# Performance work log

Measured on AMD Instinct MI355X. Metric: run time of the kernel, lower is better.

Reference implementation:

```python
import jax, jax.numpy as jnp
import numpy as np

B, T, C = 128, 384, 256
H, KV, D = 4, 2, 64          # n_head, n_kv_head, head_dim
REP = H // KV                # query heads per kv head
BLOCK_SIZE = 384


def setup_inputs() -> dict:
    key = jax.random.key(0)
    k0, k1, k2, k3, k4 = jax.random.split(key, 5)
    scale = 0.02
    return {
        "x":  jax.random.normal(k0, (B, T, C), jnp.float32),
        "Wq": jax.random.normal(k1, (C, H * D), jnp.float32) * scale,
        "Wk": jax.random.normal(k2, (C, KV * D), jnp.float32) * scale,
        "Wv": jax.random.normal(k3, (C, KV * D), jnp.float32) * scale,
        "Wo": jax.random.normal(k4, (C, C), jnp.float32) * scale,
    }


def _rope_tables(t_len):
    inv_freq = 1.0 / (10000.0 ** (jnp.arange(0, D, 2, dtype=jnp.float32) / D))
    t = jnp.arange(t_len, dtype=jnp.float32)
    freqs = jnp.outer(t, inv_freq)            # [T, D/2]
    emb = jnp.concatenate([freqs, freqs], -1)  # [T, D]
    return jnp.cos(emb), jnp.sin(emb)


def _rotate_half(x):
    h = x.shape[-1] // 2
    return jnp.concatenate([-x[..., h:], x[..., :h]], -1)


def _apply_rope(x, cos, sin):
    # x: [B, heads, T, D]; cos/sin: [T, D]
    return x * cos[None, None] + _rotate_half(x) * sin[None, None]


def reference(x, Wq, Wk, Wv, Wo):
    b, t, c = x.shape
    q = (x @ Wq).reshape(b, t, H, D).transpose(0, 2, 1, 3)   # [B,H,T,D]
    k = (x @ Wk).reshape(b, t, KV, D).transpose(0, 2, 1, 3)  # [B,KV,T,D]
    v = (x @ Wv).reshape(b, t, KV, D).transpose(0, 2, 1, 3)

    cos, sin = _rope_tables(t)
    q = _apply_rope(q, cos, sin)
    k = _apply_rope(k, cos, sin)

    # GQA: group query heads by kv head instead of repeat_interleave on K/V.
    qg = q.reshape(b, KV, REP, t, D)
    scores = jnp.einsum('bgrtd,bgsd->bgrts', qg, k) / jnp.sqrt(jnp.float32(D))
    causal = jnp.tril(jnp.ones((t, t), dtype=bool))
    scores = jnp.where(causal, scores, jnp.finfo(scores.dtype).min)
    p = jax.nn.softmax(scores, axis=-1)
    y = jnp.einsum('bgrts,bgsd->bgrtd', p, v)                 # [B,KV,REP,T,D]
    y = y.reshape(b, H, t, D).transpose(0, 2, 1, 3).reshape(b, t, c)
    return y @ Wo
```

## Files before the change

### kernel.cpp

```cpp
#include <hip/hip_runtime.h>
#include <hip/hip_bf16.h>

#define BB 128
#define TT 384
#define CC 256
#define HH 4
#define KVH 2
#define QKVW 512
#define MROWS (BB * TT)

typedef __attribute__((ext_vector_type(8))) short short8;
typedef __attribute__((ext_vector_type(4))) float float4v;

__device__ __forceinline__ unsigned short f2b(float f) {
    union { float f; unsigned u; } v; v.f = f;
    unsigned u = v.u;
    unsigned r = (u + 0x7fffu + ((u >> 16) & 1u)) >> 16;
    return (unsigned short)r;
}
__device__ __forceinline__ float4v mfma16(short8 a, short8 b, float4v c) {
    return __builtin_amdgcn_mfma_f32_16x16x32_bf16(a, b, c, 0, 0, 0);
}
__device__ __forceinline__ void g2lds16(const void* g, void* l) {
    __builtin_amdgcn_global_load_lds(
        (const __attribute__((address_space(1))) unsigned int*)g,
        (__attribute__((address_space(3))) unsigned int*)l, 16, 0, 0);
}
__device__ __forceinline__ unsigned pk2bf(float a, float b) {
    union { float f; unsigned u; } x, y; x.f = a; y.f = b;
    return __builtin_amdgcn_perm(y.u + 0x8000u, x.u + 0x8000u, 0x07060302u);
}

__global__ void prep_kernel(const float* __restrict__ Wq, const float* __restrict__ Wk,
                            const float* __restrict__ Wv, const float* __restrict__ Wo,
                            unsigned short* __restrict__ WqkvT, unsigned short* __restrict__ WoT,
                            float* __restrict__ cosT, float* __restrict__ sinT) {
    int idx = blockIdx.x * 256 + threadIdx.x;
    const int N1 = QKVW * CC;
    const int N2 = N1 + CC * CC;
    const int N3 = N2 + TT * 32;
    if (idx < N1) {
        int n = idx >> 8, k = idx & 255;
        float w;
        if (n < 256)      w = Wq[k * 256 + n];
        else if (n < 384) w = Wk[k * 128 + (n - 256)];
        else              w = Wv[k * 128 + (n - 384)];
        WqkvT[n * 256 + k] = f2b(w);
    } else if (idx < N2) {
        int i = idx - N1; int n = i >> 8, k = i & 255;
        WoT[n * 256 + k] = f2b(Wo[k * 256 + n]);
    } else if (idx < N3) {
        int i = idx - N2;
        int t = i >> 5, f = i & 31;
        double invf = exp2(-(double)f / 32.0 * 13.287712379549449);
        double ang = (double)t * invf;
        cosT[t * 32 + f] = (float)cos(ang);
        sinT[t * 32 + f] = (float)sin(ang);
    }
}

__global__ __launch_bounds__(256) void gemm_qkv_kernel(
    const float* __restrict__ X, const unsigned short* __restrict__ BT,
    unsigned short* __restrict__ Qr, unsigned short* __restrict__ Kr,
    unsigned short* __restrict__ Vt,
    const float* __restrict__ cosT, const float* __restrict__ sinT)
{
    __shared__ __align__(16) unsigned short As[2][128 * 32];
    __shared__ __align__(16) unsigned short Bs[2][128 * 32];
    const int tid  = threadIdx.x;
    const int lane = tid & 63;
    const int quad = lane >> 4, l16 = lane & 15;
    const int wave = tid >> 6;
    const int mt = ((blockIdx.x >> 5) << 3) | (blockIdx.x & 7);
    const int nt = (blockIdx.x >> 3) & 3;
    const int mbase = mt * 128, nbase = nt * 128;
    const int wmb = (wave >> 1) * 64, wnb = (wave & 1) * 64;

    float4v acc[4][4] = {};
    const int r0 = tid >> 2, kc = (tid & 3) * 8;
    const int ldsW = (tid & ~63) * 16;
    const float*          gX0 = X  + (size_t)(mbase + r0) * CC + kc;
    const unsigned short* gB0 = BT + (size_t)(nbase + r0) * CC + kc;

    float4 a0, a1, a2, a3;
    auto loadA = [&](int kt) {
        const float4* p0 = (const float4*)(gX0 + kt);
        const float4* p1 = (const float4*)(gX0 + kt + (size_t)64 * CC);
        a0 = p0[0]; a1 = p0[1]; a2 = p1[0]; a3 = p1[1];
    };
    auto writeA = [&](int bi) {
        short8 w0, w1;
        w0[0]=(short)f2b(a0.x); w0[1]=(short)f2b(a0.y); w0[2]=(short)f2b(a0.z); w0[3]=(short)f2b(a0.w);
        w0[4]=(short)f2b(a1.x); w0[5]=(short)f2b(a1.y); w0[6]=(short)f2b(a1.z); w0[7]=(short)f2b(a1.w);
        w1[0]=(short)f2b(a2.x); w1[1]=(short)f2b(a2.y); w1[2]=(short)f2b(a2.z); w1[3]=(short)f2b(a2.w);
        w1[4]=(short)f2b(a3.x); w1[5]=(short)f2b(a3.y); w1[6]=(short)f2b(a3.z); w1[7]=(short)f2b(a3.w);
        *(short8*)&As[bi][r0 * 32 + kc]        = w0;
        *(short8*)&As[bi][(r0 + 64) * 32 + kc] = w1;
    };
    auto stageB = [&](int bi, int kt) {
        g2lds16(gB0 + kt,                  (char*)&Bs[bi][0] + ldsW);
        g2lds16(gB0 + kt + (size_t)64*CC,  (char*)&Bs[bi][0] + 4096 + ldsW);
    };

    loadA(0);
    stageB(0, 0);
    writeA(0);
    for (int ks = 0; ks < 8; ks++) {
        __syncthreads();
        if (ks < 7) { loadA((ks + 1) * 32); stageB((ks + 1) & 1, (ks + 1) * 32); }
        const unsigned short* Ac = &As[ks & 1][0];
        const unsigned short* Bc = &Bs[ks & 1][0];

        short8 af[4], bf_[4];
        #pragma unroll
        for (int i = 0; i < 4; i++)
            af[i] = *(const short8*)&Ac[(wmb + i * 16 + l16) * 32 + quad * 8];
        #pragma unroll
        for (int i = 0; i < 4; i++)
            bf_[i] = *(const short8*)&Bc[(wnb + i * 16 + l16) * 32 + quad * 8];
        #pragma unroll
        for (int i = 0; i < 4; i++)
            #pragma unroll
            for (int j = 0; j < 4; j++)
                acc[i][j] = mfma16(af[i], bf_[j], acc[i][j]);

        if (ks < 7) writeA((ks + 1) & 1);
    }

    const int gn0 = nbase + wnb;
    const int gm0 = mbase + wmb;
    if (gn0 < 384) {
        const bool isq = (gn0 < 256);
        const int  hh  = isq ? (gn0 >> 6) : ((gn0 - 256) >> 6);
        const float qs = isq ? 0.18033688011112042f : 1.0f;
        #pragma unroll
        for (int i = 0; i < 4; i++) {
            #pragma unroll
            for (int r = 0; r < 4; r++) {
                int gm = gm0 + i * 16 + quad * 4 + r;
                int b = gm / TT, t = gm - b * TT;
                unsigned short* dst = isq
                    ? (Qr + (((size_t)b * HH  + hh) * TT + t) * 64)
                    : (Kr + (((size_t)b * KVH + hh) * TT + t) * 64);
                #pragma unroll
                for (int j = 0; j < 2; j++) {
                    int f = j * 16 + l16;
                    float cs = cosT[t * 32 + f], sn = sinT[t * 32 + f];
                    float a  = acc[i][j][r],     c2 = acc[i][j + 2][r];
                    dst[f]      = f2b((a * cs - c2 * sn) * qs);
                    dst[f + 32] = f2b((c2 * cs + a * sn) * qs);
                }
            }
        }
    } else {
        const int g = (gn0 - 384) >> 6;
        #pragma unroll
        for (int i = 0; i < 4; i++) {
            #pragma unroll
            for (int r = 0; r < 4; r++) {
                int gm = gm0 + i * 16 + quad * 4 + r;
                int b = gm / TT, s = gm - b * TT;
                int s6 = s & 63;
                int sig = (s6 & 15) * 4 + (s6 >> 4);
                unsigned short* dst = Vt + (((size_t)b * KVH + g) * 6 + (s >> 6)) * 4096 + sig;
                #pragma unroll
                for (int j = 0; j < 4; j++)
                    dst[(j * 16 + l16) * 64] = f2b(acc[i][j][r]);
            }
        }
    }
}

__global__ __launch_bounds__(256) void gemm_out_kernel(
    const unsigned short* __restrict__ A, const unsigned short* __restrict__ BT,
    float* __restrict__ C)
{
    __shared__ __align__(16) unsigned short As[2][128 * 32];
    __shared__ __align__(16) unsigned short Bs[2][128 * 32];
    const int tid  = threadIdx.x;
    const int lane = tid & 63;
    const int quad = lane >> 4, l16 = lane & 15;
    const int wave = tid >> 6;
    const int mt = ((blockIdx.x >> 4) << 3) | (blockIdx.x & 7);
    const int nt = (blockIdx.x >> 3) & 1;
    const int mbase = mt * 128, nbase = nt * 128;
    const int wmb = (wave >> 1) * 64, wnb = (wave & 1) * 64;

    float4v acc[4][4] = {};
    const int r0 = tid >> 2, kc = (tid & 3) * 8;
    const int ldsW = (tid & ~63) * 16;
    const unsigned short* gA0 = A  + (size_t)(mbase + r0) * CC + kc;
    const unsigned short* gB0 = BT + (size_t)(nbase + r0) * CC + kc;

    auto stage = [&](int bi, int kt) {
        g2lds16(gA0 + kt,                  (char*)&As[bi][0] + ldsW);
        g2lds16(gA0 + kt + (size_t)64*CC,  (char*)&As[bi][0] + 4096 + ldsW);
        g2lds16(gB0 + kt,                  (char*)&Bs[bi][0] + ldsW);
        g2lds16(gB0 + kt + (size_t)64*CC,  (char*)&Bs[bi][0] + 4096 + ldsW);
    };

    stage(0, 0);
    for (int ks = 0; ks < 8; ks++) {
        __syncthreads();
        if (ks < 7) stage((ks + 1) & 1, (ks + 1) * 32);
        const unsigned short* Ac = &As[ks & 1][0];
        const unsigned short* Bc = &Bs[ks & 1][0];

        short8 af[4], bf_[4];
        #pragma unroll
        for (int i = 0; i < 4; i++)
            af[i] = *(const short8*)&Ac[(wmb + i * 16 + l16) * 32 + quad * 8];
        #pragma unroll
        for (int i = 0; i < 4; i++)
            bf_[i] = *(const short8*)&Bc[(wnb + i * 16 + l16) * 32 + quad * 8];
        #pragma unroll
        for (int i = 0; i < 4; i++)
            #pragma unroll
            for (int j = 0; j < 4; j++)
                acc[i][j] = mfma16(af[i], bf_[j], acc[i][j]);
    }
    #pragma unroll
    for (int i = 0; i < 4; i++)
        #pragma unroll
        for (int j = 0; j < 4; j++)
            #pragma unroll
            for (int r = 0; r < 4; r++)
                C[(size_t)(mbase + wmb + i * 16 + quad * 4 + r) * CC + nbase + wnb + j * 16 + l16]
                    = acc[i][j][r];
}

__global__ __launch_bounds__(256, 3) void attn_kernel(
    const unsigned short* __restrict__ Qr, const unsigned short* __restrict__ Kr,
    const unsigned short* __restrict__ Vt, unsigned short* __restrict__ y)
{
    __shared__ __align__(16) unsigned short Ks[2][64 * 64];
    __shared__ __align__(16) unsigned short Vs[2][64 * 64];
    __shared__ __align__(16) unsigned short Ps[4][32 * 64];

    const int tid  = threadIdx.x;
    const int lane = tid & 63;
    const int wave = tid >> 6;
    const int quad = lane >> 4, l16 = lane & 15;

    const int xc  = blockIdx.x & 7;
    const int jj  = blockIdx.x >> 3;
    const int p   = jj % 3;
    const int bg  = (jj / 3) * 8 + xc;
    const int g   = bg & 1, b = bg >> 1;
    const int h   = g * 2 + (wave >> 1);

    const unsigned short* Kbase = Kr + ((size_t)b * KVH + g) * TT * 64;
    const unsigned short* Vbase = Vt + ((size_t)b * KVH + g) * 6 * 4096;
    const unsigned short* Qbase = Qr + ((size_t)b * HH + h) * TT * 64;
    unsigned short* ybase = y + (size_t)b * TT * CC + h * 64;
    char* Pw = (char*)&Ps[wave][0];
    const int ldsWave = (tid & ~63) * 16;
    int gc0, gc1;
    { int L0 = tid;       gc0 = ((L0 & ~7) | ((L0 & 7) ^ ((L0 >> 3) & 7))) * 8;
      int L1 = 256 + tid; gc1 = ((L1 & ~7) | ((L1 & 7) ^ ((L1 >> 3) & 7))) * 8; }

    auto stage = [&](int bi, int kt) {
        const unsigned short* kB = Kbase + (size_t)kt * 4096;
        const unsigned short* vB = Vbase + (size_t)kt * 4096;
        g2lds16(kB + gc0, (char*)&Ks[bi][0] + ldsWave);
        g2lds16(kB + gc1, (char*)&Ks[bi][0] + 4096 + ldsWave);
        g2lds16(vB + gc0, (char*)&Vs[bi][0] + ldsWave);
        g2lds16(vB + gc1, (char*)&Vs[bi][0] + 4096 + ldsWave);
    };

    short8 ones;
    #pragma unroll
    for (int j = 0; j < 8; j++) ones[j] = (short)0x3F80;

    int seq = 0;
    stage(0, 0);

    for (int tph = 0; tph < 2; tph++) {
        const int qt = tph ? (5 - p) : p;
        const int qb = qt * 64 + (wave & 1) * 32;

        short8 qf[2][2];
        #pragma unroll
        for (int mi = 0; mi < 2; mi++)
            #pragma unroll
            for (int half = 0; half < 2; half++)
                qf[mi][half] = *(const short8*)(Qbase
                    + (size_t)(qb + mi * 16 + l16) * 64 + half * 32 + quad * 8);

        float4v acc[2][4] = {};
        float4v accl[2]   = {};

        for (int kt = 0; kt <= qt; kt++) {
            __syncthreads();
            if (kt < qt)        stage((seq + 1) & 1, kt + 1);
            else if (tph == 0)  stage((seq + 1) & 1, 0);
            const unsigned short* Kc = &Ks[seq & 1][0];
            const unsigned short* Vc = &Vs[seq & 1][0];

            float4v s_[2][4];
            #pragma unroll
            for (int js = 0; js < 4; js++) {
                int srow = js * 16 + l16, sw = srow & 7;
                short8 kb0 = *(const short8*)((const char*)Kc + srow * 128 + ((quad ^ sw) * 16));
                short8 kb1 = *(const short8*)((const char*)Kc + srow * 128 + (((4 + quad) ^ sw) * 16));
                #pragma unroll
                for (int mi = 0; mi < 2; mi++) {
                    float4v z = {};
                    z = mfma16(qf[mi][0], kb0, z);
                    s_[mi][js] = mfma16(qf[mi][1], kb1, z);
                }
            }

            if (kt == qt) {
                #pragma unroll
                for (int mi = 0; mi < 2; mi++)
                    #pragma unroll
                    for (int js = 0; js < 4; js++) {
                        int coll = js * 16 + l16;
                        #pragma unroll
                        for (int r = 0; r < 4; r++) {
                            int rowl = (wave & 1) * 32 + mi * 16 + quad * 4 + r;
                            if (coll > rowl) s_[mi][js][r] = -1e30f;
                        }
                    }
            }

            #pragma unroll
            for (int mi = 0; mi < 2; mi++)
                #pragma unroll
                for (int r = 0; r < 4; r++) {
                    float e0 = __builtin_amdgcn_exp2f(s_[mi][0][r]);
                    float e1 = __builtin_amdgcn_exp2f(s_[mi][1][r]);
                    float e2 = __builtin_amdgcn_exp2f(s_[mi][2][r]);
                    float e3 = __builtin_amdgcn_exp2f(s_[mi][3][r]);
                    unsigned long long d =
                        (unsigned long long)pk2bf(e0, e1) |
                        ((unsigned long long)pk2bf(e2, e3) << 32);
                    int rho = mi * 16 + quad * 4 + r;
                    int ch  = l16 ^ (((quad * 4 + r) & 7) << 1);
                    *(unsigned long long*)(Pw + rho * 128 + ch * 8) = d;
                }

            short8 pa[2][2];
            #pragma unroll
            for (int mi = 0; mi < 2; mi++)
                #pragma unroll
                for (int half = 0; half < 2; half++) {
                    int chp = (2 * (half * 4 + quad)) ^ ((l16 & 7) << 1);
                    pa[mi][half] = *(const short8*)(Pw + (mi * 16 + l16) * 128 + chp * 8);
                }
            #pragma unroll
            for (int dj = 0; dj < 4; dj++) {
                int vrow = dj * 16 + l16, sw = vrow & 7;
                short8 vb0 = *(const short8*)((const char*)Vc + vrow * 128 + ((quad ^ sw) * 16));
                short8 vb1 = *(const short8*)((const char*)Vc + vrow * 128 + (((4 + quad) ^ sw) * 16));
                #pragma unroll
                for (int mi = 0; mi < 2; mi++) {
                    acc[mi][dj] = mfma16(pa[mi][0], vb0, acc[mi][dj]);
                    acc[mi][dj] = mfma16(pa[mi][1], vb1, acc[mi][dj]);
                }
            }
            #pragma unroll
            for (int mi = 0; mi < 2; mi++) {
                accl[mi] = mfma16(pa[mi][0], ones, accl[mi]);
                accl[mi] = mfma16(pa[mi][1], ones, accl[mi]);
            }
            seq++;
        }

        #pragma unroll
        for (int mi = 0; mi < 2; mi++) {
            float rinv[4];
            #pragma unroll
            for (int r = 0; r < 4; r++) rinv[r] = 1.0f / accl[mi][r];
            #pragma unroll
            for (int dj = 0; dj < 4; dj++)
                #pragma unroll
                for (int r = 0; r < 4; r++) {
                    int tt = qb + mi * 16 + quad * 4 + r;
                    ybase[(size_t)tt * CC + dj * 16 + l16] = f2b(acc[mi][dj][r] * rinv[r]);
                }
        }
    }
}

extern "C" void kernel_launch(void* const* d_in, const int* in_sizes, int n_in,
                              void* d_out, int out_size, void* d_ws, size_t ws_size,
                              hipStream_t stream) {
    const float* x  = (const float*)d_in[0];
    const float* Wq = (const float*)d_in[1];
    const float* Wk = (const float*)d_in[2];
    const float* Wv = (const float*)d_in[3];
    const float* Wo = (const float*)d_in[4];
    float* out = (float*)d_out;

    char* ws = (char*)d_ws;
    size_t off = 0;
    unsigned short* Qr = (unsigned short*)(ws + off); off += (size_t)BB * HH  * TT * 64 * 2;
    unsigned short* Kr = (unsigned short*)(ws + off); off += (size_t)BB * KVH * TT * 64 * 2;
    unsigned short* Vt = (unsigned short*)(ws + off); off += (size_t)BB * KVH * TT * 64 * 2;
    unsigned short* y  = (unsigned short*)(ws + off); off += (size_t)MROWS * CC * 2;
    unsigned short* WqkvT = (unsigned short*)(ws + off); off += (size_t)QKVW * CC * 2;
    unsigned short* WoT   = (unsigned short*)(ws + off); off += (size_t)CC * CC * 2;
    float* cosT = (float*)(ws + off); off += (size_t)TT * 32 * 4;
    float* sinT = (float*)(ws + off); off += (size_t)TT * 32 * 4;

    prep_kernel<<<816, 256, 0, stream>>>(Wq, Wk, Wv, Wo, WqkvT, WoT, cosT, sinT);
    gemm_qkv_kernel<<<(MROWS / 128) * 4, 256, 0, stream>>>(x, WqkvT, Qr, Kr, Vt, cosT, sinT);
    attn_kernel<<<BB * KVH * 3, 256, 0, stream>>>(Qr, Kr, Vt, y);
    gemm_out_kernel<<<(MROWS / 128) * 2, 256, 0, stream>>>(y, WoT, out);
}
```

Before: 165.1 us.

## Stage V-transpose epilogue through swizzled LDS and prefetch A two steps ahead

Before, the V projection output was written to its transposed layout with scattered 2-byte global stores. Now it is first packed into a per-wave swizzled LDS tile, then written out as coalesced 16-byte rows, reusing the main-loop shared buffer. The A operand (fp32 X) also gets a second register stage, so global loads are issued two k-steps ahead. This costs extra registers, plus block-wide barriers in the V epilogue.

```diff
diff --git a/kernel.cpp b/kernel.cpp
--- a/kernel.cpp
+++ b/kernel.cpp
@@ -65,8 +65,7 @@
     unsigned short* __restrict__ Vt,
     const float* __restrict__ cosT, const float* __restrict__ sinT)
 {
-    __shared__ __align__(16) unsigned short As[2][128 * 32];
-    __shared__ __align__(16) unsigned short Bs[2][128 * 32];
+    __shared__ __align__(16) unsigned short SH[16384];
     const int tid  = threadIdx.x;
     const int lane = tid & 63;
     const int quad = lane >> 4, l16 = lane & 15;
@@ -82,34 +81,37 @@
     const float*          gX0 = X  + (size_t)(mbase + r0) * CC + kc;
     const unsigned short* gB0 = BT + (size_t)(nbase + r0) * CC + kc;
 
-    float4 a0, a1, a2, a3;
-    auto loadA = [&](int kt) {
+    float4 ar[2][4];
+    auto loadA = [&](int st, int kt) {
         const float4* p0 = (const float4*)(gX0 + kt);
         const float4* p1 = (const float4*)(gX0 + kt + (size_t)64 * CC);
-        a0 = p0[0]; a1 = p0[1]; a2 = p1[0]; a3 = p1[1];
+        ar[st][0] = p0[0]; ar[st][1] = p0[1]; ar[st][2] = p1[0]; ar[st][3] = p1[1];
     };
-    auto writeA = [&](int bi) {
+    auto writeA = [&](int bi, int st) {
         short8 w0, w1;
-        w0[0]=(short)f2b(a0.x); w0[1]=(short)f2b(a0.y); w0[2]=(short)f2b(a0.z); w0[3]=(short)f2b(a0.w);
-        w0[4]=(short)f2b(a1.x); w0[5]=(short)f2b(a1.y); w0[6]=(short)f2b(a1.z); w0[7]=(short)f2b(a1.w);
-        w1[0]=(short)f2b(a2.x); w1[1]=(short)f2b(a2.y); w1[2]=(short)f2b(a2.z); w1[3]=(short)f2b(a2.w);
-        w1[4]=(short)f2b(a3.x); w1[5]=(short)f2b(a3.y); w1[6]=(short)f2b(a3.z); w1[7]=(short)f2b(a3.w);
-        *(short8*)&As[bi][r0 * 32 + kc]        = w0;
-        *(short8*)&As[bi][(r0 + 64) * 32 + kc] = w1;
+        w0[0]=(short)f2b(ar[st][0].x); w0[1]=(short)f2b(ar[st][0].y); w0[2]=(short)f2b(ar[st][0].z); w0[3]=(short)f2b(ar[st][0].w);
+        w0[4]=(short)f2b(ar[st][1].x); w0[5]=(short)f2b(ar[st][1].y); w0[6]=(short)f2b(ar[st][1].z); w0[7]=(short)f2b(ar[st][1].w);
+        w1[0]=(short)f2b(ar[st][2].x); w1[1]=(short)f2b(ar[st][2].y); w1[2]=(short)f2b(ar[st][2].z); w1[3]=(short)f2b(ar[st][2].w);
+        w1[4]=(short)f2b(ar[st][3].x); w1[5]=(short)f2b(ar[st][3].y); w1[6]=(short)f2b(ar[st][3].z); w1[7]=(short)f2b(ar[st][3].w);
+        *(short8*)&SH[bi * 4096 + r0 * 32 + kc]        = w0;
+        *(short8*)&SH[bi * 4096 + (r0 + 64) * 32 + kc] = w1;
     };
     auto stageB = [&](int bi, int kt) {
-        g2lds16(gB0 + kt,                  (char*)&Bs[bi][0] + ldsW);
-        g2lds16(gB0 + kt + (size_t)64*CC,  (char*)&Bs[bi][0] + 4096 + ldsW);
+        g2lds16(gB0 + kt,                  (char*)SH + 16384 + bi * 8192 + ldsW);
+        g2lds16(gB0 + kt + (size_t)64*CC,  (char*)SH + 16384 + bi * 8192 + 4096 + ldsW);
     };
 
-    loadA(0);
+    loadA(0, 0);
     stageB(0, 0);
-    writeA(0);
+    loadA(1, 32);
+    writeA(0, 0);
+    #pragma unroll
     for (int ks = 0; ks < 8; ks++) {
         __syncthreads();
-        if (ks < 7) { loadA((ks + 1) * 32); stageB((ks + 1) & 1, (ks + 1) * 32); }
-        const unsigned short* Ac = &As[ks & 1][0];
-        const unsigned short* Bc = &Bs[ks & 1][0];
+        if (ks < 6) loadA(ks & 1, (ks + 2) * 32);
+        if (ks < 7) stageB((ks + 1) & 1, (ks + 1) * 32);
+        const unsigned short* Ac = &SH[(ks & 1) * 4096];
+        const unsigned short* Bc = &SH[8192 + (ks & 1) * 4096];
 
         short8 af[4], bf_[4];
         #pragma unroll
@@ -124,7 +126,7 @@
             for (int j = 0; j < 4; j++)
                 acc[i][j] = mfma16(af[i], bf_[j], acc[i][j]);
 
-        if (ks < 7) writeA((ks + 1) & 1);
+        if (ks < 7) writeA((ks + 1) & 1, (ks + 1) & 1);
     }
 
     const int gn0 = nbase + wnb;
@@ -153,20 +155,34 @@
             }
         }
     } else {
-        const int g = (gn0 - 384) >> 6;
-        #pragma unroll
-        for (int i = 0; i < 4; i++) {
+        const int gq = (gn0 - 384) >> 6;
+        const int bb = (mbase + wmb) / TT;
+        const int tl = ((mbase + wmb) % TT) >> 6;
+        unsigned short* Tw = &SH[wave * 4096];
+        __syncthreads();
+        #pragma unroll
+        for (int j = 0; j < 4; j++) {
+            int dl = j * 16 + l16;
+            int xr = (dl & 7) << 3;
             #pragma unroll
             for (int r = 0; r < 4; r++) {
-                int gm = gm0 + i * 16 + quad * 4 + r;
-                int b = gm / TT, s = gm - b * TT;
-                int s6 = s & 63;
-                int sig = (s6 & 15) * 4 + (s6 >> 4);
-                unsigned short* dst = Vt + (((size_t)b * KVH + g) * 6 + (s >> 6)) * 4096 + sig;
-                #pragma unroll
-                for (int j = 0; j < 4; j++)
-                    dst[(j * 16 + l16) * 64] = f2b(acc[i][j][r]);
-            }
+                #pragma unroll
+                for (int ip = 0; ip < 2; ip++) {
+                    unsigned v = (unsigned)f2b(acc[2 * ip][j][r])
+                               | ((unsigned)f2b(acc[2 * ip + 1][j][r]) << 16);
+                    int sigp = (quad * 4 + r) * 4 + 2 * ip;
+                    *(unsigned*)(Tw + dl * 64 + (sigp ^ xr)) = v;
+                }
+            }
+        }
+        __syncthreads();
+        unsigned short* dstb = Vt + (((size_t)bb * KVH + gq) * 6 + tl) * 4096;
+        const int c = lane & 7;
+        #pragma unroll
+        for (int it = 0; it < 8; it++) {
+            int d = it * 8 + (lane >> 3);
+            short8 v = *(const short8*)(Tw + d * 64 + (c << 3));
+            *(short8*)(dstb + (size_t)d * 64 + ((c ^ (d & 7)) << 3)) = v;
         }
     }
 }
```

Result: no change. 164.3 us (-0.5%).
